# Kernel optimization log

Hardware: AMD Instinct MI355X
Metric: run time of the kernel (lower is better)

Reference implementation:

```python
import jax, jax.numpy as jnp
import numpy as np

EMBED_DIM = 768
NUM_HEADS = 12
HEAD_DIM = EMBED_DIM // NUM_HEADS
SCALE = HEAD_DIM ** -0.5


def setup_inputs() -> dict:
    key = jax.random.key(0)
    ks = jax.random.split(key, 9)
    B, S, D = 2, 2048, EMBED_DIM
    init = 1.0 / np.sqrt(D)  # ~ nn.Linear default uniform scale
    x = jax.random.normal(ks[0], (B, S, D), dtype=jnp.float32)
    Wq = jax.random.uniform(ks[1], (D, D), jnp.float32, -init, init)
    bq = jax.random.uniform(ks[2], (D,), jnp.float32, -init, init)
    Wk = jax.random.uniform(ks[3], (D, D), jnp.float32, -init, init)
    bk = jax.random.uniform(ks[4], (D,), jnp.float32, -init, init)
    Wv = jax.random.uniform(ks[5], (D, D), jnp.float32, -init, init)
    bv = jax.random.uniform(ks[6], (D,), jnp.float32, -init, init)
    Wo = jax.random.uniform(ks[7], (D, D), jnp.float32, -init, init)
    bo = jax.random.uniform(ks[8], (D,), jnp.float32, -init, init)
    return {"x": x, "Wq": Wq, "bq": bq, "Wk": Wk, "bk": bk,
            "Wv": Wv, "bv": bv, "Wo": Wo, "bo": bo}


def reference(x, Wq, bq, Wk, bk, Wv, bv, Wo, bo):
    B, S, D = x.shape
    H, Dh = NUM_HEADS, HEAD_DIM
    # projections; weights stored as (in, out) so x @ W == torch Linear with W.T
    q = (x @ Wq + bq).reshape(B, S, H, Dh).transpose(0, 2, 1, 3)  # [B,H,S,Dh]
    k = (x @ Wk + bk).reshape(B, S, H, Dh).transpose(0, 2, 1, 3)
    v = (x @ Wv + bv).reshape(B, S, H, Dh).transpose(0, 2, 1, 3)
    scores = jnp.einsum("bhqd,bhkd->bhqk", q, k) * SCALE        # [B,H,S,S]
    weights = jax.nn.softmax(scores, axis=-1)
    out = jnp.einsum("bhqk,bhkd->bhqd", weights, v)              # [B,H,S,Dh]
    out = out.transpose(0, 2, 1, 3).reshape(B, S, D)
    return out @ Wo + bo
```

## Files before the change

kernel.cpp:

```cpp
#include <hip/hip_runtime.h>
#include <math.h>

#define BB 2
#define SS 2048
#define DDIM 768
#define HH 12
#define DH 64
#define NROWS (BB*SS)
#define NQT2 (SS/128)

typedef _Float16 f16;
typedef _Float16 half2v __attribute__((ext_vector_type(2)));
typedef __fp16 fp16x2 __attribute__((ext_vector_type(2)));
typedef _Float16 half4 __attribute__((ext_vector_type(4)));
typedef _Float16 half8 __attribute__((ext_vector_type(8)));
typedef float f32x4 __attribute__((ext_vector_type(4)));

__device__ __forceinline__ half2v cvt_pk_f16(float a, float b) {
    fp16x2 t = __builtin_amdgcn_cvt_pkrtz(a, b);
    return __builtin_bit_cast(half2v, t);
}

#define MFMA16(a,b,c) __builtin_amdgcn_mfma_f32_16x16x32_f16((a),(b),(c),0,0,0)
#define QSCALE (0.125f * 1.44269504088896f)
#define M_STATIC 10.0f

__device__ __forceinline__ int swz(int row, int chunk16) {
    return row*128 + ((chunk16 ^ (row & 7)) << 4);
}

__global__ __launch_bounds__(256) void prep_w(const float* __restrict__ Wq, const float* __restrict__ Wk,
                                              const float* __restrict__ Wv, const float* __restrict__ Wo,
                                              f16* __restrict__ Wt)
{
    const int z = blockIdx.z;
    const float* W = z==0 ? Wq : (z==1 ? Wk : (z==2 ? Wv : Wo));
    f16* out = Wt + (size_t)z * DDIM * DDIM;

    __shared__ float tile[64][65];
    const int t = threadIdx.x;
    const int k0 = blockIdx.x*64, n0 = blockIdx.y*64;

    const int kr = t >> 2, nc = (t & 3) * 16;
    #pragma unroll
    for (int i = 0; i < 4; ++i) {
        float4 v = *(const float4*)&W[(size_t)(k0+kr)*DDIM + n0 + nc + i*4];
        tile[kr][nc+i*4+0] = v.x; tile[kr][nc+i*4+1] = v.y;
        tile[kr][nc+i*4+2] = v.z; tile[kr][nc+i*4+3] = v.w;
    }
    __syncthreads();
    const int nr = t >> 2, kc = (t & 3) * 16;
    half8 h0, h1;
    #pragma unroll
    for (int j = 0; j < 8; ++j) {
        h0[j] = (f16)tile[kc + j][nr];
        h1[j] = (f16)tile[kc + 8 + j][nr];
    }
    *(half8*)&out[(size_t)(n0+nr)*DDIM + k0 + kc]     = h0;
    *(half8*)&out[(size_t)(n0+nr)*DDIM + k0 + kc + 8] = h1;
}

__global__ __launch_bounds__(256) void proj_qkv(const float* __restrict__ x, const f16* __restrict__ Wt,
        const float* __restrict__ bq, const float* __restrict__ bk, const float* __restrict__ bv,
        f16* __restrict__ qb, f16* __restrict__ kb2, f16* __restrict__ vtb)
{
    const int z = blockIdx.z;
    const f16* Wz = Wt + (size_t)z * DDIM * DDIM;
    const float* bias = z==0 ? bq : (z==1 ? bk : bv);
    const float qscale = (z==0) ? QSCALE : 1.0f;

    __shared__ __align__(16) unsigned char lds[64*1024];

    const int tid = threadIdx.x;
    const int l = tid & 63, w = tid >> 6;
    const int g = l >> 4, qi = l & 15;
    const int wm = w >> 1, wn = w & 1;
    const int m0 = blockIdx.x * 128, n0 = blockIdx.y * 128;

    f32x4 acc[4][4];
    #pragma unroll
    for (int i=0;i<4;i++)
        #pragma unroll
        for (int j=0;j<4;j++) { f32x4 zv = {0.f,0.f,0.f,0.f}; acc[i][j] = zv; }

    half8 sa[4], sb[4];

#define GLOAD(t) { \
        _Pragma("unroll") \
        for (int i = 0; i < 4; ++i) { \
            int c = i*256 + tid, row = c >> 3, kc = c & 7; \
            const float* xp = &x[(size_t)(m0+row)*DDIM + (t)*64 + kc*8]; \
            float4 a0 = *(const float4*)xp; \
            float4 a1 = *(const float4*)(xp + 4); \
            half8 hv = {(f16)a0.x,(f16)a0.y,(f16)a0.z,(f16)a0.w, \
                        (f16)a1.x,(f16)a1.y,(f16)a1.z,(f16)a1.w}; \
            sa[i] = hv; \
            sb[i] = *(const half8*)&Wz[(size_t)(n0+row)*DDIM + (t)*64 + kc*8]; \
        } }

#define GWRT(bufi) { \
        unsigned char* As_ = lds + (bufi)*32768; \
        unsigned char* Bs_ = As_ + 16384; \
        _Pragma("unroll") \
        for (int i = 0; i < 4; ++i) { \
            int c = i*256 + tid, row = c >> 3, kc = c & 7; \
            *(half8*)(As_ + swz(row, kc)) = sa[i]; \
            *(half8*)(Bs_ + swz(row, kc)) = sb[i]; \
        } }

    GLOAD(0); GWRT(0);
    __syncthreads();

    for (int t = 0; t < 12; ++t) {
        const int cur = t & 1;
        if (t < 11) GLOAD(t+1);

        const unsigned char* As = lds + cur*32768;
        const unsigned char* Bs = As + 16384;

        half8 af[4][2], bf[4][2];
        #pragma unroll
        for (int mt = 0; mt < 4; ++mt) {
            int row = wm*64 + mt*16 + qi;
            #pragma unroll
            for (int kh = 0; kh < 2; ++kh)
                af[mt][kh] = *(const half8*)(As + swz(row, kh*4 + g));
        }
        #pragma unroll
        for (int nt = 0; nt < 4; ++nt) {
            int row = wn*64 + nt*16 + qi;
            #pragma unroll
            for (int kh = 0; kh < 2; ++kh)
                bf[nt][kh] = *(const half8*)(Bs + swz(row, kh*4 + g));
        }
        __builtin_amdgcn_s_setprio(1);
        #pragma unroll
        for (int mt = 0; mt < 4; ++mt)
            #pragma unroll
            for (int nt = 0; nt < 4; ++nt) {
                acc[mt][nt] = MFMA16(af[mt][0], bf[nt][0], acc[mt][nt]);
                acc[mt][nt] = MFMA16(af[mt][1], bf[nt][1], acc[mt][nt]);
            }
        __builtin_amdgcn_s_setprio(0);

        if (t < 11) GWRT(cur^1);
        __syncthreads();
    }

    if (z == 2) {
        #pragma unroll
        for (int mt = 0; mt < 4; ++mt)
            #pragma unroll
            for (int nt = 0; nt < 4; ++nt) {
                int m = m0 + wm*64 + mt*16 + g*4;
                int n = n0 + wn*64 + nt*16 + qi;
                int b = m >> 11, s = m & 2047;
                int h = n >> 6,  d = n & 63;
                float bs = bias[n];
                half4 o4 = {(f16)(acc[mt][nt][0] + bs), (f16)(acc[mt][nt][1] + bs),
                            (f16)(acc[mt][nt][2] + bs), (f16)(acc[mt][nt][3] + bs)};
                *(half4*)&vtb[(((size_t)(b*HH + h))*DH + d)*SS + s] = o4;
            }
    } else {
        f16* out = (z == 0) ? qb : kb2;
        #pragma unroll
        for (int mt = 0; mt < 4; ++mt)
            #pragma unroll
            for (int nt = 0; nt < 4; ++nt)
                #pragma unroll
                for (int r = 0; r < 4; ++r) {
                    int m = m0 + wm*64 + mt*16 + g*4 + r;
                    int n = n0 + wn*64 + nt*16 + qi;
                    float v = (acc[mt][nt][r] + bias[n]) * qscale;
                    int b = m >> 11, s = m & 2047;
                    int h = n >> 6,  d = n & 63;
                    out[(((size_t)(b*HH + h))*SS + s)*DH + d] = (f16)v;
                }
    }
#undef GLOAD
#undef GWRT
}

__global__ __launch_bounds__(256) void attn_mfma(
        const f16* __restrict__ qbuf, const f16* __restrict__ kbuf,
        const f16* __restrict__ vtbuf, f16* __restrict__ pO, float* __restrict__ mlb)
{
    __shared__ __align__(16) unsigned char lds[48*1024];

    const int tid = threadIdx.x;
    const int l = tid & 63, w = tid >> 6;
    const int g = l >> 4, qi = l & 15;
    const int qt = blockIdx.x, h = blockIdx.y;
    const int b = blockIdx.z >> 1, khalf = blockIdx.z & 1;
    const int q0 = qt * 128 + w * 32;
    const size_t base = ((size_t)(b * HH + h)) * SS * DH;
    const int key0 = khalf * (SS/2);
    const int pid = (b * HH + h) * NQT2 + qt;

    unsigned char* Pw = lds + 32768 + w*4096;

    half8 qf[2][2];
    #pragma unroll
    for (int f = 0; f < 2; ++f)
        #pragma unroll
        for (int kh = 0; kh < 2; ++kh)
            qf[f][kh] = *(const half8*)&qbuf[base + (size_t)(q0 + f*16 + qi)*DH + kh*32 + g*8];

    f32x4 oacc[2][4];
    #pragma unroll
    for (int f = 0; f < 2; ++f)
        #pragma unroll
        for (int i = 0; i < 4; ++i) { f32x4 zv = {0.f,0.f,0.f,0.f}; oacc[f][i] = zv; }
    float lsum[2] = {0.f, 0.f};
    const f32x4 minit = {-M_STATIC, -M_STATIC, -M_STATIC, -M_STATIC};

    half8 sk[2], svv[2];

#define LOADT(t) { \
        _Pragma("unroll") \
        for (int i = 0; i < 2; ++i) { \
            int c = i*256 + tid, row = c >> 3, col = c & 7; \
            sk[i]  = *(const half8*)&kbuf[base + (size_t)(key0 + (t)*64 + row)*DH + col*8]; \
            svv[i] = *(const half8*)&vtbuf[base + (size_t)row*SS + key0 + (t)*64 + col*8]; \
        } }

#define WRT(bufi) { \
        unsigned char* Kw_ = lds + (bufi)*16384; \
        unsigned char* Vw_ = Kw_ + 8192; \
        _Pragma("unroll") \
        for (int i = 0; i < 2; ++i) { \
            int c = i*256 + tid, row = c >> 3, col = c & 7; \
            *(half8*)(Kw_ + swz(row, col)) = sk[i]; \
            *(half8*)(Vw_ + swz(row, col)) = svv[i]; \
        } }

    LOADT(0); WRT(0);
    __syncthreads();

    for (int t = 0; t < 16; ++t) {
        const int cur = t & 1;
        if (t < 15) LOADT(t+1);

        const unsigned char* Kb = lds + cur*16384;
        const unsigned char* Vb = Kb + 8192;

        half8 kf[8];
        #pragma unroll
        for (int mt = 0; mt < 4; ++mt)
            #pragma unroll
            for (int kh = 0; kh < 2; ++kh)
                kf[mt*2+kh] = *(const half8*)(Kb + swz(mt*16 + qi, kh*4 + g));
        half8 vf[8];
        #pragma unroll
        for (int dt = 0; dt < 4; ++dt)
            #pragma unroll
            for (int kh = 0; kh < 2; ++kh)
                vf[dt*2+kh] = *(const half8*)(Vb + swz(dt*16 + qi, kh*4 + g));

        #pragma unroll
        for (int f = 0; f < 2; ++f) {
            f32x4 sv[4];
            __builtin_amdgcn_s_setprio(1);
            #pragma unroll
            for (int mt = 0; mt < 4; ++mt) {
                f32x4 zz = MFMA16(kf[mt*2+0], qf[f][0], minit);
                sv[mt] = MFMA16(kf[mt*2+1], qf[f][1], zz);
            }
            __builtin_amdgcn_s_setprio(0);
            half2v ph[8];
            #pragma unroll
            for (int mt = 0; mt < 4; ++mt) {
                float e0 = exp2f(sv[mt][0]);
                float e1 = exp2f(sv[mt][1]);
                float e2 = exp2f(sv[mt][2]);
                float e3 = exp2f(sv[mt][3]);
                ph[mt*2+0] = cvt_pk_f16(e0, e1);
                ph[mt*2+1] = cvt_pk_f16(e2, e3);
                half4 pk = {ph[mt*2+0][0], ph[mt*2+0][1], ph[mt*2+1][0], ph[mt*2+1][1]};
                *(half4*)(Pw + swz(f*16 + qi, 2*mt + (g>>1)) + (g&1)*8) = pk;
            }
            half2v s01 = (ph[0] + ph[1]) + (ph[2] + ph[3]);
            half2v s23 = (ph[4] + ph[5]) + (ph[6] + ph[7]);
            half2v st = s01 + s23;
            float rs = (float)st[0] + (float)st[1];
            rs += __shfl_xor(rs, 16);
            rs += __shfl_xor(rs, 32);
            lsum[f] += rs;
        }

        #pragma unroll
        for (int f = 0; f < 2; ++f) {
            half8 pf0 = *(const half8*)(Pw + swz(f*16 + qi, g));
            half8 pf1 = *(const half8*)(Pw + swz(f*16 + qi, 4 + g));
            __builtin_amdgcn_s_setprio(1);
            #pragma unroll
            for (int dt = 0; dt < 4; ++dt) {
                oacc[f][dt] = MFMA16(vf[dt*2+0], pf0, oacc[f][dt]);
                oacc[f][dt] = MFMA16(vf[dt*2+1], pf1, oacc[f][dt]);
            }
            __builtin_amdgcn_s_setprio(0);
        }

        if (t < 15) WRT(cur^1);
        __syncthreads();
    }

    f16* po = pO + ((size_t)pid*2 + khalf) * (128*64);
    float* mlp = mlb + ((size_t)pid*2 + khalf) * 128;
    #pragma unroll
    for (int f = 0; f < 2; ++f) {
        const int qw = w*32 + f*16 + qi;
        const float inv = 1.0f / lsum[f];
        #pragma unroll
        for (int dt = 0; dt < 4; ++dt) {
            half4 o4 = {(f16)(oacc[f][dt][0]*inv), (f16)(oacc[f][dt][1]*inv),
                        (f16)(oacc[f][dt][2]*inv), (f16)(oacc[f][dt][3]*inv)};
            *(half4*)&po[qw*64 + dt*16 + g*4] = o4;
        }
        if (g == 0) mlp[qw] = lsum[f];
    }
#undef LOADT
#undef WRT
}

__global__ __launch_bounds__(256) void proj_out(const f16* __restrict__ pO, const float* __restrict__ mlb,
                                                const f16* __restrict__ Wt, const float* __restrict__ bo,
                                                float* __restrict__ out)
{
    const f16* Wz = Wt + (size_t)3 * DDIM * DDIM;

    __shared__ __align__(16) unsigned char lds[64*1024];

    const int tid = threadIdx.x;
    const int l = tid & 63, w = tid >> 6;
    const int g = l >> 4, qi = l & 15;
    const int wm = w >> 1, wn = w & 1;
    const int m0 = blockIdx.x * 128, n0 = blockIdx.y * 128;

    f32x4 acc[4][4];
    #pragma unroll
    for (int i=0;i<4;i++)
        #pragma unroll
        for (int j=0;j<4;j++) { f32x4 zv = {0.f,0.f,0.f,0.f}; acc[i][j] = zv; }

    half8 sa[4], sb[4];

#define GLOAD(t) { \
        _Pragma("unroll") \
        for (int i = 0; i < 4; ++i) { \
            int c = i*256 + tid, row = c >> 3, kc = c & 7; \
            int m = m0 + row, bb_ = m >> 11, ss_ = m & 2047; \
            int qt_ = ss_ >> 7, qr_ = ss_ & 127; \
            int pid_ = (bb_*HH + (t))*NQT2 + qt_; \
            const f16* P0_ = pO + ((size_t)pid_*2 + 0)*(128*64) + qr_*64 + kc*8; \
            const f16* P1_ = pO + ((size_t)pid_*2 + 1)*(128*64) + qr_*64 + kc*8; \
            half8 xv = *(const half8*)P0_; \
            half8 yv = *(const half8*)P1_; \
            float l0 = mlb[((size_t)pid_*2 + 0)*128 + qr_]; \
            float l1 = mlb[((size_t)pid_*2 + 1)*128 + qr_]; \
            float winv = 1.0f / (l0 + l1); \
            float w0 = l0 * winv, w1 = l1 * winv; \
            half8 rv; \
            _Pragma("unroll") \
            for (int j = 0; j < 8; ++j) \
                rv[j] = (f16)(w0*(float)xv[j] + w1*(float)yv[j]); \
            sa[i] = rv; \
            sb[i] = *(const half8*)&Wz[(size_t)(n0+row)*DDIM + (t)*64 + kc*8]; \
        } }

#define GWRT(bufi) { \
        unsigned char* As_ = lds + (bufi)*32768; \
        unsigned char* Bs_ = As_ + 16384; \
        _Pragma("unroll") \
        for (int i = 0; i < 4; ++i) { \
            int c = i*256 + tid, row = c >> 3, kc = c & 7; \
            *(half8*)(As_ + swz(row, kc)) = sa[i]; \
            *(half8*)(Bs_ + swz(row, kc)) = sb[i]; \
        } }

    GLOAD(0); GWRT(0);
    __syncthreads();

    for (int t = 0; t < 12; ++t) {
        const int cur = t & 1;
        if (t < 11) GLOAD(t+1);

        const unsigned char* As = lds + cur*32768;
        const unsigned char* Bs = As + 16384;

        half8 af[4][2], bf[4][2];
        #pragma unroll
        for (int mt = 0; mt < 4; ++mt) {
            int row = wm*64 + mt*16 + qi;
            #pragma unroll
            for (int kh = 0; kh < 2; ++kh)
                af[mt][kh] = *(const half8*)(As + swz(row, kh*4 + g));
        }
        #pragma unroll
        for (int nt = 0; nt < 4; ++nt) {
            int row = wn*64 + nt*16 + qi;
            #pragma unroll
            for (int kh = 0; kh < 2; ++kh)
                bf[nt][kh] = *(const half8*)(Bs + swz(row, kh*4 + g));
        }
        __builtin_amdgcn_s_setprio(1);
        #pragma unroll
        for (int mt = 0; mt < 4; ++mt)
            #pragma unroll
            for (int nt = 0; nt < 4; ++nt) {
                acc[mt][nt] = MFMA16(af[mt][0], bf[nt][0], acc[mt][nt]);
                acc[mt][nt] = MFMA16(af[mt][1], bf[nt][1], acc[mt][nt]);
            }
        __builtin_amdgcn_s_setprio(0);

        if (t < 11) GWRT(cur^1);
        __syncthreads();
    }

    #pragma unroll
    for (int mt = 0; mt < 4; ++mt)
        #pragma unroll
        for (int nt = 0; nt < 4; ++nt)
            #pragma unroll
            for (int r = 0; r < 4; ++r) {
                int m = m0 + wm*64 + mt*16 + g*4 + r;
                int n = n0 + wn*64 + nt*16 + qi;
                out[(size_t)m*DDIM + n] = acc[mt][nt][r] + bo[n];
            }
#undef GLOAD
#undef GWRT
}

extern "C" void kernel_launch(void* const* d_in, const int* in_sizes, int n_in,
                              void* d_out, int out_size, void* d_ws, size_t ws_size,
                              hipStream_t stream)
{
    const float* x  = (const float*)d_in[0];
    const float* Wq = (const float*)d_in[1];
    const float* bq = (const float*)d_in[2];
    const float* Wk = (const float*)d_in[3];
    const float* bk = (const float*)d_in[4];
    const float* Wv = (const float*)d_in[5];
    const float* bv = (const float*)d_in[6];
    const float* Wo = (const float*)d_in[7];
    const float* bo = (const float*)d_in[8];

    char* ws = (char*)d_ws;
    const size_t WT_B  = (size_t)4 * DDIM * DDIM * 2;
    const size_t HB_B  = (size_t)BB * HH * SS * DH * 2;
    const size_t PO_B  = (size_t)BB * HH * NQT2 * 2 * 128 * 64 * 2;

    f16* Wt = (f16*)ws;
    f16* qb = (f16*)(ws + WT_B);
    f16* kb = (f16*)(ws + WT_B + HB_B);
    f16* vt = (f16*)(ws + WT_B + 2*HB_B);
    f16* pO = (f16*)(ws + WT_B + 3*HB_B);
    float* mlb = (float*)(ws + WT_B + 3*HB_B + PO_B);

    prep_w<<<dim3(DDIM/64, DDIM/64, 4), 256, 0, stream>>>(Wq, Wk, Wv, Wo, Wt);
    proj_qkv<<<dim3(NROWS/128, DDIM/128, 3), 256, 0, stream>>>(x, Wt, bq, bk, bv, qb, kb, vt);
    attn_mfma<<<dim3(NQT2, HH, BB*2), 256, 0, stream>>>(qb, kb, vt, pO, mlb);
    proj_out<<<dim3(NROWS/128, DDIM/128), 256, 0, stream>>>(pO, mlb, Wt, bo, (float*)d_out);
}
```

Baseline: 120.3 us.

## Switch attention to 32x32x16 MFMA and pass P via permlane32 swap instead of LDS

Rewrites the attention inner loop to use 32x32x16 MFMA tiles instead of 16x16x32. The S^T output layout can then be turned into the B operand of the PV MFMA with v_permlane32_swap, so the per-wave LDS round trip for P is removed and the LDS allocation drops from 48KB to 32KB. This removes LDS writes and reads of P, cuts the row-sum shuffle from two steps to one, and may raise occupancy. In exchange it relies on exact lane/register layout correspondence, and the 16-element accumulators raise register pressure.

```diff
diff --git a/kernel.cpp b/kernel.cpp
--- a/kernel.cpp
+++ b/kernel.cpp
@@ -15,6 +15,9 @@
 typedef _Float16 half4 __attribute__((ext_vector_type(4)));
 typedef _Float16 half8 __attribute__((ext_vector_type(8)));
 typedef float f32x4 __attribute__((ext_vector_type(4)));
+typedef float f32x16 __attribute__((ext_vector_type(16)));
+typedef unsigned int u32;
+typedef unsigned int u32x4v __attribute__((ext_vector_type(4)));
 
 __device__ __forceinline__ half2v cvt_pk_f16(float a, float b) {
     fp16x2 t = __builtin_amdgcn_cvt_pkrtz(a, b);
@@ -22,6 +25,7 @@
 }
 
 #define MFMA16(a,b,c) __builtin_amdgcn_mfma_f32_16x16x32_f16((a),(b),(c),0,0,0)
+#define MFMA32(a,b,c) __builtin_amdgcn_mfma_f32_32x32x16_f16((a),(b),(c),0,0,0)
 #define QSCALE (0.125f * 1.44269504088896f)
 #define M_STATIC 10.0f
 
@@ -185,11 +189,11 @@
         const f16* __restrict__ qbuf, const f16* __restrict__ kbuf,
         const f16* __restrict__ vtbuf, f16* __restrict__ pO, float* __restrict__ mlb)
 {
-    __shared__ __align__(16) unsigned char lds[48*1024];
+    __shared__ __align__(16) unsigned char lds[32*1024];
 
     const int tid = threadIdx.x;
     const int l = tid & 63, w = tid >> 6;
-    const int g = l >> 4, qi = l & 15;
+    const int q31 = l & 31, hl = l >> 5;
     const int qt = blockIdx.x, h = blockIdx.y;
     const int b = blockIdx.z >> 1, khalf = blockIdx.z & 1;
     const int q0 = qt * 128 + w * 32;
@@ -197,22 +201,20 @@
     const int key0 = khalf * (SS/2);
     const int pid = (b * HH + h) * NQT2 + qt;
 
-    unsigned char* Pw = lds + 32768 + w*4096;
-
-    half8 qf[2][2];
-    #pragma unroll
-    for (int f = 0; f < 2; ++f)
-        #pragma unroll
-        for (int kh = 0; kh < 2; ++kh)
-            qf[f][kh] = *(const half8*)&qbuf[base + (size_t)(q0 + f*16 + qi)*DH + kh*32 + g*8];
-
-    f32x4 oacc[2][4];
-    #pragma unroll
-    for (int f = 0; f < 2; ++f)
-        #pragma unroll
-        for (int i = 0; i < 4; ++i) { f32x4 zv = {0.f,0.f,0.f,0.f}; oacc[f][i] = zv; }
-    float lsum[2] = {0.f, 0.f};
-    const f32x4 minit = {-M_STATIC, -M_STATIC, -M_STATIC, -M_STATIC};
+    half8 qf[4];
+    #pragma unroll
+    for (int s = 0; s < 4; ++s)
+        qf[s] = *(const half8*)&qbuf[base + (size_t)(q0 + q31)*DH + s*16 + hl*8];
+
+    f32x16 oacc[2];
+    #pragma unroll
+    for (int dt = 0; dt < 2; ++dt)
+        #pragma unroll
+        for (int i = 0; i < 16; ++i) oacc[dt][i] = 0.f;
+    float lsum = 0.f;
+    f32x16 minit16;
+    #pragma unroll
+    for (int i = 0; i < 16; ++i) minit16[i] = -M_STATIC;
 
     half8 sk[2], svv[2];
 
@@ -244,62 +246,64 @@
         const unsigned char* Kb = lds + cur*16384;
         const unsigned char* Vb = Kb + 8192;
 
-        half8 kf[8];
-        #pragma unroll
-        for (int mt = 0; mt < 4; ++mt)
-            #pragma unroll
-            for (int kh = 0; kh < 2; ++kh)
-                kf[mt*2+kh] = *(const half8*)(Kb + swz(mt*16 + qi, kh*4 + g));
-        half8 vf[8];
-        #pragma unroll
-        for (int dt = 0; dt < 4; ++dt)
-            #pragma unroll
-            for (int kh = 0; kh < 2; ++kh)
-                vf[dt*2+kh] = *(const half8*)(Vb + swz(dt*16 + qi, kh*4 + g));
-
-        #pragma unroll
-        for (int f = 0; f < 2; ++f) {
-            f32x4 sv[4];
+        half8 kA[2][4];
+        #pragma unroll
+        for (int mt = 0; mt < 2; ++mt)
+            #pragma unroll
+            for (int s = 0; s < 4; ++s)
+                kA[mt][s] = *(const half8*)(Kb + swz(mt*32 + q31, 2*s + hl));
+        half8 vA[2][4];
+        #pragma unroll
+        for (int dt = 0; dt < 2; ++dt)
+            #pragma unroll
+            for (int ks = 0; ks < 4; ++ks)
+                vA[dt][ks] = *(const half8*)(Vb + swz(dt*32 + q31, 2*ks + hl));
+
+        half2v ph[16];
+        #pragma unroll
+        for (int mt = 0; mt < 2; ++mt) {
             __builtin_amdgcn_s_setprio(1);
-            #pragma unroll
-            for (int mt = 0; mt < 4; ++mt) {
-                f32x4 zz = MFMA16(kf[mt*2+0], qf[f][0], minit);
-                sv[mt] = MFMA16(kf[mt*2+1], qf[f][1], zz);
-            }
+            f32x16 sv = minit16;
+            #pragma unroll
+            for (int s = 0; s < 4; ++s)
+                sv = MFMA32(kA[mt][s], qf[s], sv);
             __builtin_amdgcn_s_setprio(0);
-            half2v ph[8];
-            #pragma unroll
-            for (int mt = 0; mt < 4; ++mt) {
-                float e0 = exp2f(sv[mt][0]);
-                float e1 = exp2f(sv[mt][1]);
-                float e2 = exp2f(sv[mt][2]);
-                float e3 = exp2f(sv[mt][3]);
-                ph[mt*2+0] = cvt_pk_f16(e0, e1);
-                ph[mt*2+1] = cvt_pk_f16(e2, e3);
-                half4 pk = {ph[mt*2+0][0], ph[mt*2+0][1], ph[mt*2+1][0], ph[mt*2+1][1]};
-                *(half4*)(Pw + swz(f*16 + qi, 2*mt + (g>>1)) + (g&1)*8) = pk;
-            }
-            half2v s01 = (ph[0] + ph[1]) + (ph[2] + ph[3]);
-            half2v s23 = (ph[4] + ph[5]) + (ph[6] + ph[7]);
-            half2v st = s01 + s23;
-            float rs = (float)st[0] + (float)st[1];
-            rs += __shfl_xor(rs, 16);
+            #pragma unroll
+            for (int r = 0; r < 16; r += 2)
+                ph[mt*8 + (r>>1)] = cvt_pk_f16(exp2f(sv[r]), exp2f(sv[r+1]));
+        }
+
+        {
+            half2v t01 = (ph[0]+ph[1]) + (ph[2]+ph[3]);
+            half2v t23 = (ph[4]+ph[5]) + (ph[6]+ph[7]);
+            half2v t45 = (ph[8]+ph[9]) + (ph[10]+ph[11]);
+            half2v t67 = (ph[12]+ph[13]) + (ph[14]+ph[15]);
+            half2v tt = (t01+t23) + (t45+t67);
+            float rs = (float)tt[0] + (float)tt[1];
             rs += __shfl_xor(rs, 32);
-            lsum[f] += rs;
-        }
-
-        #pragma unroll
-        for (int f = 0; f < 2; ++f) {
-            half8 pf0 = *(const half8*)(Pw + swz(f*16 + qi, g));
-            half8 pf1 = *(const half8*)(Pw + swz(f*16 + qi, 4 + g));
-            __builtin_amdgcn_s_setprio(1);
-            #pragma unroll
-            for (int dt = 0; dt < 4; ++dt) {
-                oacc[f][dt] = MFMA16(vf[dt*2+0], pf0, oacc[f][dt]);
-                oacc[f][dt] = MFMA16(vf[dt*2+1], pf1, oacc[f][dt]);
-            }
-            __builtin_amdgcn_s_setprio(0);
-        }
+            lsum += rs;
+        }
+
+        half8 pf[4];
+        #pragma unroll
+        for (int ks = 0; ks < 4; ++ks) {
+            u32 x0 = __builtin_bit_cast(u32, ph[4*ks + 0]);
+            u32 x2 = __builtin_bit_cast(u32, ph[4*ks + 2]);
+            asm volatile("v_permlane32_swap_b32 %0, %1" : "+v"(x0), "+v"(x2));
+            u32 x1 = __builtin_bit_cast(u32, ph[4*ks + 1]);
+            u32 x3 = __builtin_bit_cast(u32, ph[4*ks + 3]);
+            asm volatile("v_permlane32_swap_b32 %0, %1" : "+v"(x1), "+v"(x3));
+            u32x4v tv = {x0, x1, x2, x3};
+            pf[ks] = __builtin_bit_cast(half8, tv);
+        }
+
+        __builtin_amdgcn_s_setprio(1);
+        #pragma unroll
+        for (int dt = 0; dt < 2; ++dt)
+            #pragma unroll
+            for (int ks = 0; ks < 4; ++ks)
+                oacc[dt] = MFMA32(vA[dt][ks], pf[ks], oacc[dt]);
+        __builtin_amdgcn_s_setprio(0);
 
         if (t < 15) WRT(cur^1);
         __syncthreads();
@@ -307,18 +311,17 @@
 
     f16* po = pO + ((size_t)pid*2 + khalf) * (128*64);
     float* mlp = mlb + ((size_t)pid*2 + khalf) * 128;
-    #pragma unroll
-    for (int f = 0; f < 2; ++f) {
-        const int qw = w*32 + f*16 + qi;
-        const float inv = 1.0f / lsum[f];
-        #pragma unroll
-        for (int dt = 0; dt < 4; ++dt) {
-            half4 o4 = {(f16)(oacc[f][dt][0]*inv), (f16)(oacc[f][dt][1]*inv),
-                        (f16)(oacc[f][dt][2]*inv), (f16)(oacc[f][dt][3]*inv)};
-            *(half4*)&po[qw*64 + dt*16 + g*4] = o4;
-        }
-        if (g == 0) mlp[qw] = lsum[f];
-    }
+    const int qw = w*32 + q31;
+    const float inv = 1.0f / lsum;
+    #pragma unroll
+    for (int dt = 0; dt < 2; ++dt)
+        #pragma unroll
+        for (int g2 = 0; g2 < 4; ++g2) {
+            half4 o4 = {(f16)(oacc[dt][g2*4+0]*inv), (f16)(oacc[dt][g2*4+1]*inv),
+                        (f16)(oacc[dt][g2*4+2]*inv), (f16)(oacc[dt][g2*4+3]*inv)};
+            *(half4*)&po[qw*64 + dt*32 + g2*8 + hl*4] = o4;
+        }
+    if (hl == 0) mlp[qw] = lsum;
 #undef LOADT
 #undef WRT
 }
```

New measurement: 118.4 us. Within noise of the previous version (-1.6%).
